# Kernel optimization log

Hardware: AMD Instinct MI355X
Metric: run time of the kernel (lower is better)

The kernel has to match this reference:

```python
import jax, jax.numpy as jnp
import numpy as np

N_Q = 16384; N_S = 16384; NN = 32; F_IN = 128; F_OUT = 256
K = 15; DIM = 3
RADIUS = 10.0
KP_EXTENT_CFG = 1.0      # config.NETWORK.KP_EXTENT (also scales learned offsets)
DENSITY = 5.0            # config.NETWORK.DENSITY_PARAMETER
EXTENT = KP_EXTENT_CFG * RADIUS / DENSITY   # 2.0
K_RADIUS = 1.5 * EXTENT
OFFSET_DIM = DIM * (K - 1)  # modulated=False, version=0 -> 42


def setup_inputs() -> dict:
    key = jax.random.key(0)
    ks = jax.random.split(key, 8)
    query_points = jax.random.uniform(ks[0], (N_Q, DIM), dtype=jnp.float32)
    support_points = jax.random.uniform(ks[1], (N_S, DIM), dtype=jnp.float32)
    neighbors = jax.random.randint(ks[2], (N_Q, NN), 0, N_S)
    features = jax.random.normal(ks[3], (N_S, F_IN), dtype=jnp.float32)
    # kernel points: fixed disposition inside ball of radius 1.5*extent, first point at center
    kp = jax.random.normal(ks[4], (K, DIM), dtype=jnp.float32)
    kp = kp / jnp.linalg.norm(kp, axis=1, keepdims=True) * (0.7 * K_RADIUS)
    K_points = kp.at[0].set(0.0)
    weight = jax.random.normal(ks[5], (K, F_IN, F_OUT), dtype=jnp.float32) / np.sqrt(F_IN)
    deformable_weight = jax.random.normal(ks[6], (K, F_IN, OFFSET_DIM), dtype=jnp.float32) / np.sqrt(F_IN)
    bias = jnp.zeros((OFFSET_DIM,), dtype=jnp.float32)
    return {"query_points": query_points, "support_points": support_points,
            "neighbors": neighbors, "features": features, "K_points": K_points,
            "weight": weight, "deformable_weight": deformable_weight, "bias": bias}


def _gather_neighb(query_points, support_points, neighbors, features):
    # pad with shadow point (far away) and zero feature row, as in KPConv_ops
    sp = jnp.concatenate([support_points, jnp.full((1, DIM), 1e6, support_points.dtype)], 0)
    ft = jnp.concatenate([features, jnp.zeros((1, features.shape[1]), features.dtype)], 0)
    rel = sp[neighbors] - query_points[:, None, :]   # [n, nn, 3]
    nfeat = ft[neighbors]                            # [n, nn, f]
    return rel, nfeat


def _linear_influence(sq_dist):
    # KP_INFLUENCE='linear': relu(1 - d/extent); CONVOLUTION_MODE='sum'
    return jnp.maximum(1.0 - jnp.sqrt(sq_dist) / EXTENT, 0.0)


def reference(query_points, support_points, neighbors, features, K_points,
              weight, deformable_weight, bias):
    rel, nfeat = _gather_neighb(query_points, support_points, neighbors, features)

    # --- rigid KPConv producing offsets (version=0) ---
    d0 = rel[:, :, None, :] - K_points[None, None, :, :]   # [n, nn, K, 3]
    sq0 = jnp.sum(d0 * d0, axis=-1)                        # [n, nn, K]
    w0 = _linear_influence(sq0)
    wf0 = jnp.einsum('enk,enf->ekf', w0, nfeat)            # [n, K, f]
    feat0 = jnp.einsum('ekf,kfo->eo', wf0, deformable_weight) + bias  # [n, 42]

    # not modulated: reshape to offsets, prepend zero offset for center kernel point
    offsets = feat0.reshape(-1, K - 1, DIM)
    offsets = jnp.concatenate([jnp.zeros_like(offsets[:, :1, :]), offsets], axis=1)
    offsets = offsets * KP_EXTENT_CFG                      # [n, K, 3]

    # --- deformable KPConv ---
    def_kp = K_points[None, :, :] + offsets                # [n, K, 3]
    d1 = rel[:, :, None, :] - def_kp[:, None, :, :]        # [n, nn, K, 3]
    sq1 = jnp.sum(d1 * d1, axis=-1)                        # [n, nn, K]
    w1 = _linear_influence(sq1)                            # out-of-range neighbors get 0 weight
    wf1 = jnp.einsum('enk,enf->ekf', w1, nfeat)            # [n, K, f]
    out = jnp.einsum('ekf,kfo->eo', wf1, weight)           # [n, f_out]
    return out
```

## Files before the change

kernel.cpp:

```cpp
#include <hip/hip_runtime.h>
#include <hip/hip_bf16.h>
#include <math.h>

typedef __attribute__((ext_vector_type(8))) short bf16x8;
typedef __attribute__((ext_vector_type(4))) float f32x4;

#define NQ 16384
#define NN 32
#define FI 128
#define FO 256
#define KPN 15
#define OD 42
#define INV_EXT 0.5f

#define KT2 64
#define WFA_STRIDE 2056

#define WS_DEFKP  0u
#define WS_FEATBF (3u * 1024u * 1024u)
#define WS_BSW    (7u * 1024u * 1024u)
#define WS_DWBH   (8u * 1024u * 1024u)
#define WS_DWBL   (WS_DWBH + 196608u)
#define WS_FEATPK (9u * 1024u * 1024u)

static __device__ __forceinline__ unsigned short f2bf(float x) {
    union { __hip_bfloat16 h; unsigned short u; } cv;
    cv.h = __float2bfloat16(x);
    return cv.u;
}
static __device__ __forceinline__ float bf2f(unsigned short h) {
    union { unsigned int u; float f; } cv;
    cv.u = ((unsigned int)h) << 16;
    return cv.f;
}

__global__ void prep_feat(const float* __restrict__ in,
                          unsigned short* __restrict__ fbf,
                          unsigned int* __restrict__ fpk) {
    const int i = (blockIdx.x * 256 + threadIdx.x) * 4;
    if (i >= NQ * FI) return;
    float4 a = *(const float4*)&in[i];
    unsigned short h0 = f2bf(a.x), h1 = f2bf(a.y), h2 = f2bf(a.z), h3 = f2bf(a.w);
    unsigned int* bp = (unsigned int*)&fbf[i];
    bp[0] = (unsigned int)h0 | ((unsigned int)h1 << 16);
    bp[1] = (unsigned int)h2 | ((unsigned int)h3 << 16);
    fpk[i + 0] = (unsigned int)h0 | ((unsigned int)f2bf(a.x - bf2f(h0)) << 16);
    fpk[i + 1] = (unsigned int)h1 | ((unsigned int)f2bf(a.y - bf2f(h1)) << 16);
    fpk[i + 2] = (unsigned int)h2 | ((unsigned int)f2bf(a.z - bf2f(h2)) << 16);
    fpk[i + 3] = (unsigned int)h3 | ((unsigned int)f2bf(a.w - bf2f(h3)) << 16);
}

__global__ void swz_B(const float* __restrict__ w, unsigned short* __restrict__ Bsw) {
    const int tid = blockIdx.x * 256 + threadIdx.x;
    const int lane = tid & 63;
    const int kt   = (tid >> 6) & 63;
    const int nt   = tid >> 12;
    const int n    = nt * 16 + (lane & 15);
    const int kbase = kt * 32 + (lane >> 4) * 8;
    unsigned int p[4];
    #pragma unroll
    for (int jj = 0; jj < 4; jj++) {
        unsigned int lo, hi;
        {
            const int kk = kbase + 2 * jj;
            const int f = kk >> 4, k = kk & 15;
            lo = (k < KPN) ? f2bf(w[(k * FI + f) * FO + n]) : 0u;
        }
        {
            const int kk = kbase + 2 * jj + 1;
            const int f = kk >> 4, k = kk & 15;
            hi = (k < KPN) ? f2bf(w[(k * FI + f) * FO + n]) : 0u;
        }
        p[jj] = lo | (hi << 16);
    }
    unsigned int* op = (unsigned int*)&Bsw[tid * 8];
    op[0] = p[0]; op[1] = p[1]; op[2] = p[2]; op[3] = p[3];
}

__global__ void build_dwB(const float* __restrict__ dw,
                          unsigned short* __restrict__ hi,
                          unsigned short* __restrict__ lo) {
    const int tid = blockIdx.x * 256 + threadIdx.x;
    if (tid >= 3 * 64 * 64) return;
    const int lane = tid & 63;
    const int kt   = (tid >> 6) & 63;
    const int nt   = tid >> 12;
    const int o    = nt * 16 + (lane & 15);
    const int kbase = kt * 32 + (lane >> 4) * 8;
    #pragma unroll
    for (int j = 0; j < 8; j++) {
        const int kf = kbase + j;
        const int f = kf >> 4, k = kf & 15;
        float v = (k < KPN && o < OD) ? dw[(k * FI + f) * OD + o] : 0.f;
        unsigned short h = f2bf(v);
        hi[tid * 8 + j] = h;
        lo[tid * 8 + j] = f2bf(v - bf2f(h));
    }
}

__global__ __launch_bounds__(512, 4)
void k1_offsets(const float* __restrict__ query, const float* __restrict__ support,
                const int* __restrict__ neighbors, const unsigned int* __restrict__ featpk,
                const float* __restrict__ kpoints,
                const unsigned short* __restrict__ dwB_hi,
                const unsigned short* __restrict__ dwB_lo,
                const float* __restrict__ bias, float* __restrict__ defkp)
{
    __shared__ unsigned short wfA_hi[8 * WFA_STRIDE];
    __shared__ unsigned short wfA_lo[8 * WFA_STRIDE];
    __shared__ float relx[256], rely[256], relz[256];
    __shared__ int   nbr_s[256];
    __shared__ float kp_s[48];
    __shared__ f32x4 cred[3 * 64];

    const int t = threadIdx.x;
    const int qbase = blockIdx.x * 8;
    if (t < 45) kp_s[t] = kpoints[t];
    if (t >= 45 && t < 48) kp_s[t] = 0.f;

    if (t < 256) {
        const int e = t >> 5, n = t & 31;
        const int q = qbase + e;
        const int idx = neighbors[q * NN + n];
        nbr_s[t] = idx;
        relx[t] = support[idx * 3 + 0] - query[q * 3 + 0];
        rely[t] = support[idx * 3 + 1] - query[q * 3 + 1];
        relz[t] = support[idx * 3 + 2] - query[q * 3 + 2];
    }
    __syncthreads();

    const int wave = t >> 6, lane = t & 63;
    const int quad = lane >> 4, low = lane & 15;

    {
        const int ee = wave;
        const int kb = (low < KPN) ? low * 3 : 0;
        const float kx = kp_s[kb + 0], ky = kp_s[kb + 1], kz = kp_s[kb + 2];
        union { unsigned short u[8]; bf16x8 v; } ah, al;
        int rows[8];
        #pragma unroll
        for (int j = 0; j < 8; j++) {
            const int ni = ee * 32 + quad * 8 + j;
            rows[j] = nbr_s[ni];
            const float dx = relx[ni] - kx;
            const float dy = rely[ni] - ky;
            const float dz = relz[ni] - kz;
            const float d = sqrtf(dx * dx + dy * dy + dz * dz);
            float w = 1.0f - d * INV_EXT;
            w = (low < KPN && w > 0.f) ? w : 0.f;
            const unsigned short h = f2bf(w);
            ah.u[j] = h;
            al.u[j] = f2bf(w - bf2f(h));
        }
        #pragma unroll
        for (int ft = 0; ft < 8; ft++) {
            union { unsigned int u[4]; bf16x8 v; } bh, bl;
            #pragma unroll
            for (int jj = 0; jj < 4; jj++) {
                const unsigned int d0 = featpk[rows[2 * jj] * FI + ft * 16 + low];
                const unsigned int d1 = featpk[rows[2 * jj + 1] * FI + ft * 16 + low];
                bh.u[jj] = __builtin_amdgcn_perm(d1, d0, 0x05040100u);
                bl.u[jj] = __builtin_amdgcn_perm(d1, d0, 0x07060302u);
            }
            f32x4 acc = {0.f, 0.f, 0.f, 0.f};
            acc = __builtin_amdgcn_mfma_f32_16x16x32_bf16(al.v, bh.v, acc, 0, 0, 0);
            acc = __builtin_amdgcn_mfma_f32_16x16x32_bf16(ah.v, bl.v, acc, 0, 0, 0);
            acc = __builtin_amdgcn_mfma_f32_16x16x32_bf16(ah.v, bh.v, acc, 0, 0, 0);
            const int kfb = (ft * 16 + low) * 16 + quad * 4;
            const unsigned short h0 = f2bf(acc[0]), h1 = f2bf(acc[1]);
            const unsigned short h2 = f2bf(acc[2]), h3 = f2bf(acc[3]);
            unsigned int* ph = (unsigned int*)&wfA_hi[ee * WFA_STRIDE + kfb];
            ph[0] = (unsigned int)h0 | ((unsigned int)h1 << 16);
            ph[1] = (unsigned int)h2 | ((unsigned int)h3 << 16);
            unsigned int* pl = (unsigned int*)&wfA_lo[ee * WFA_STRIDE + kfb];
            pl[0] = (unsigned int)f2bf(acc[0] - bf2f(h0)) |
                    ((unsigned int)f2bf(acc[1] - bf2f(h1)) << 16);
            pl[1] = (unsigned int)f2bf(acc[2] - bf2f(h2)) |
                    ((unsigned int)f2bf(acc[3] - bf2f(h3)) << 16);
        }
    }
    __syncthreads();

    f32x4 acc = {0.f, 0.f, 0.f, 0.f};
    const int nt = wave >> 1, half = wave & 1;
    if (wave < 6) {
        const bf16x8* Bh = (const bf16x8*)dwB_hi;
        const bf16x8* Bl = (const bf16x8*)dwB_lo;
        const int arow = (low & 7) * WFA_STRIDE;
        const int kt0 = half * 32;
        for (int kt = kt0; kt < kt0 + 32; kt++) {
            bf16x8 a_h = *(const bf16x8*)&wfA_hi[arow + kt * 32 + quad * 8];
            bf16x8 a_l = *(const bf16x8*)&wfA_lo[arow + kt * 32 + quad * 8];
            bf16x8 b_h = Bh[(nt * KT2 + kt) * 64 + lane];
            bf16x8 b_l = Bl[(nt * KT2 + kt) * 64 + lane];
            acc = __builtin_amdgcn_mfma_f32_16x16x32_bf16(a_l, b_h, acc, 0, 0, 0);
            acc = __builtin_amdgcn_mfma_f32_16x16x32_bf16(a_h, b_l, acc, 0, 0, 0);
            acc = __builtin_amdgcn_mfma_f32_16x16x32_bf16(a_h, b_h, acc, 0, 0, 0);
        }
        if (half == 1) cred[nt * 64 + lane] = acc;
    } else if (wave == 6 && lane < 24) {
        defkp[(qbase + lane / 3) * 45 + (lane % 3)] = kp_s[lane % 3];
    }
    __syncthreads();

    if (wave < 6 && half == 0) {
        f32x4 o2 = cred[nt * 64 + lane];
        acc[0] += o2[0]; acc[1] += o2[1]; acc[2] += o2[2]; acc[3] += o2[3];
        const int o = nt * 16 + low;
        if (quad < 2 && o < OD) {
            const float bo = bias[o] + kp_s[3 + o];
            #pragma unroll
            for (int r = 0; r < 4; r++) {
                const int ee = quad * 4 + r;
                defkp[(qbase + ee) * 45 + 3 + o] = bo + acc[r];
            }
        }
    }
}

__global__ __launch_bounds__(512, 4)
void k2_deform(const float* __restrict__ query, const float* __restrict__ support,
               const int* __restrict__ neighbors, const unsigned short* __restrict__ featbf,
               const unsigned short* __restrict__ Bsw, const float* __restrict__ defkp,
               float* __restrict__ out)
{
    __shared__ unsigned short wfA[16 * WFA_STRIDE];
    __shared__ float relx[512], rely[512], relz[512];
    __shared__ float dk_s[16 * 45];
    __shared__ int   nbr_s[512];

    const int t = threadIdx.x;
    const int qbase = blockIdx.x * 16;

    for (int i = t; i < 16 * 45; i += 512) dk_s[i] = defkp[qbase * 45 + i];

    const int e = t >> 5, n = t & 31;
    const int q = qbase + e;
    const int idx = neighbors[q * NN + n];
    nbr_s[t] = idx;
    relx[t] = support[idx * 3 + 0] - query[q * 3 + 0];
    rely[t] = support[idx * 3 + 1] - query[q * 3 + 1];
    relz[t] = support[idx * 3 + 2] - query[q * 3 + 2];
    __syncthreads();

    const int wave = t >> 6, lane = t & 63;
    const int quad = lane >> 4, low = lane & 15;

    {
        const int kb = (low < KPN) ? low * 3 : 0;
        for (int ei = 0; ei < 2; ei++) {
            const int ee = wave * 2 + ei;
            const float kx = dk_s[ee * 45 + kb + 0];
            const float ky = dk_s[ee * 45 + kb + 1];
            const float kz = dk_s[ee * 45 + kb + 2];
            union { unsigned short u[8]; bf16x8 v; } a;
            int rows[8];
            #pragma unroll
            for (int j = 0; j < 8; j++) {
                const int ni = ee * 32 + quad * 8 + j;
                rows[j] = nbr_s[ni];
                const float dx = relx[ni] - kx;
                const float dy = rely[ni] - ky;
                const float dz = relz[ni] - kz;
                const float d = sqrtf(dx * dx + dy * dy + dz * dz);
                float w = 1.0f - d * INV_EXT;
                w = (low < KPN && w > 0.f) ? w : 0.f;
                a.u[j] = f2bf(w);
            }
            #pragma unroll
            for (int ft = 0; ft < 8; ft++) {
                unsigned int p[4];
                #pragma unroll
                for (int j = 0; j < 4; j++) {
                    unsigned int lo2 = featbf[rows[2 * j] * FI + ft * 16 + low];
                    unsigned int hi2 = featbf[rows[2 * j + 1] * FI + ft * 16 + low];
                    p[j] = lo2 | (hi2 << 16);
                }
                bf16x8 b;
                {
                    union { unsigned int u[4]; bf16x8 v; } cv;
                    cv.u[0] = p[0]; cv.u[1] = p[1]; cv.u[2] = p[2]; cv.u[3] = p[3];
                    b = cv.v;
                }
                f32x4 acc = {0.f, 0.f, 0.f, 0.f};
                acc = __builtin_amdgcn_mfma_f32_16x16x32_bf16(a.v, b, acc, 0, 0, 0);
                const unsigned int w0 = (unsigned int)f2bf(acc[0]) | ((unsigned int)f2bf(acc[1]) << 16);
                const unsigned int w1 = (unsigned int)f2bf(acc[2]) | ((unsigned int)f2bf(acc[3]) << 16);
                unsigned short* wp = &wfA[ee * WFA_STRIDE + (ft * 16 + low) * 16 + quad * 4];
                ((unsigned int*)wp)[0] = w0;
                ((unsigned int*)wp)[1] = w1;
            }
        }
    }
    __syncthreads();

    {
        const int nt0 = wave * 2, nt1 = nt0 + 1;
        f32x4 acc0 = {0.f, 0.f, 0.f, 0.f}, acc1 = {0.f, 0.f, 0.f, 0.f};
        const bf16x8* Bp = (const bf16x8*)Bsw;
        bf16x8 a_c  = *(const bf16x8*)&wfA[low * WFA_STRIDE + quad * 8];
        bf16x8 b0_c = Bp[(nt0 * KT2) * 64 + lane];
        bf16x8 b1_c = Bp[(nt1 * KT2) * 64 + lane];
        for (int kt = 0; kt < KT2 - 1; kt++) {
            bf16x8 a_n  = *(const bf16x8*)&wfA[low * WFA_STRIDE + (kt + 1) * 32 + quad * 8];
            bf16x8 b0_n = Bp[(nt0 * KT2 + kt + 1) * 64 + lane];
            bf16x8 b1_n = Bp[(nt1 * KT2 + kt + 1) * 64 + lane];
            acc0 = __builtin_amdgcn_mfma_f32_16x16x32_bf16(a_c, b0_c, acc0, 0, 0, 0);
            acc1 = __builtin_amdgcn_mfma_f32_16x16x32_bf16(a_c, b1_c, acc1, 0, 0, 0);
            a_c = a_n; b0_c = b0_n; b1_c = b1_n;
        }
        acc0 = __builtin_amdgcn_mfma_f32_16x16x32_bf16(a_c, b0_c, acc0, 0, 0, 0);
        acc1 = __builtin_amdgcn_mfma_f32_16x16x32_bf16(a_c, b1_c, acc1, 0, 0, 0);
        #pragma unroll
        for (int r = 0; r < 4; r++) {
            const int ee = quad * 4 + r;
            out[(qbase + ee) * FO + nt0 * 16 + low] = acc0[r];
            out[(qbase + ee) * FO + nt1 * 16 + low] = acc1[r];
        }
    }
}

extern "C" void kernel_launch(void* const* d_in, const int* in_sizes, int n_in,
                              void* d_out, int out_size, void* d_ws, size_t ws_size,
                              hipStream_t stream) {
    const float* query     = (const float*)d_in[0];
    const float* support   = (const float*)d_in[1];
    const int*   neighbors = (const int*)  d_in[2];
    const float* features  = (const float*)d_in[3];
    const float* kpoints   = (const float*)d_in[4];
    const float* weight    = (const float*)d_in[5];
    const float* dweight   = (const float*)d_in[6];
    const float* bias      = (const float*)d_in[7];
    float*       out       = (float*)d_out;

    char* ws = (char*)d_ws;
    float*          defkp  = (float*)(ws + WS_DEFKP);
    unsigned short* featbf = (unsigned short*)(ws + WS_FEATBF);
    unsigned short* Bsw    = (unsigned short*)(ws + WS_BSW);
    unsigned short* dwBh   = (unsigned short*)(ws + WS_DWBH);
    unsigned short* dwBl   = (unsigned short*)(ws + WS_DWBL);
    unsigned int*   featpk = (unsigned int*)(ws + WS_FEATPK);

    prep_feat<<<(NQ * FI / 4 + 255) / 256, 256, 0, stream>>>(features, featbf, featpk);
    build_dwB<<<48, 256, 0, stream>>>(dweight, dwBh, dwBl);
    swz_B<<<256, 256, 0, stream>>>(weight, Bsw);

    k1_offsets<<<NQ / 8, 512, 0, stream>>>(query, support, neighbors, featpk,
                                           kpoints, dwBh, dwBl, bias, defkp);
    k2_deform<<<NQ / 16, 512, 0, stream>>>(query, support, neighbors, featbf,
                                           Bsw, defkp, out);
}
```

Measured before the change: 194.6 us.

## Fuse offset and deformable KPConv kernels, cache gathered features in registers

Merges the three preprocessing kernels into one launch and fuses the offset-producing KPConv with the deformable KPConv in a single kernel. Deformed kernel points stay in shared memory, and the gathered bf16 feature fragments stay in registers so the second stage does not gather them again. This removes the defkp round trip through global memory, the separate bf16 feature copy, and two launches. In exchange the fused kernel holds 32 extra registers per thread, which may hurt occupancy. The final GEMM now runs on 8 queries per block (half the MFMA rows wasted) instead of 16, which halves reuse of the B weights per block.

```diff
diff --git a/kernel.cpp b/kernel.cpp
--- a/kernel.cpp
+++ b/kernel.cpp
@@ -16,12 +16,10 @@
 #define KT2 64
 #define WFA_STRIDE 2056
 
-#define WS_DEFKP  0u
-#define WS_FEATBF (3u * 1024u * 1024u)
-#define WS_BSW    (7u * 1024u * 1024u)
-#define WS_DWBH   (8u * 1024u * 1024u)
+#define WS_FEATPK 0u
+#define WS_BSW    (8u * 1024u * 1024u)
+#define WS_DWBH   (9u * 1024u * 1024u)
 #define WS_DWBL   (WS_DWBH + 196608u)
-#define WS_FEATPK (9u * 1024u * 1024u)
 
 static __device__ __forceinline__ unsigned short f2bf(float x) {
     union { __hip_bfloat16 h; unsigned short u; } cv;
@@ -34,77 +32,72 @@
     return cv.f;
 }
 
-__global__ void prep_feat(const float* __restrict__ in,
-                          unsigned short* __restrict__ fbf,
-                          unsigned int* __restrict__ fpk) {
-    const int i = (blockIdx.x * 256 + threadIdx.x) * 4;
-    if (i >= NQ * FI) return;
-    float4 a = *(const float4*)&in[i];
-    unsigned short h0 = f2bf(a.x), h1 = f2bf(a.y), h2 = f2bf(a.z), h3 = f2bf(a.w);
-    unsigned int* bp = (unsigned int*)&fbf[i];
-    bp[0] = (unsigned int)h0 | ((unsigned int)h1 << 16);
-    bp[1] = (unsigned int)h2 | ((unsigned int)h3 << 16);
-    fpk[i + 0] = (unsigned int)h0 | ((unsigned int)f2bf(a.x - bf2f(h0)) << 16);
-    fpk[i + 1] = (unsigned int)h1 | ((unsigned int)f2bf(a.y - bf2f(h1)) << 16);
-    fpk[i + 2] = (unsigned int)h2 | ((unsigned int)f2bf(a.z - bf2f(h2)) << 16);
-    fpk[i + 3] = (unsigned int)h3 | ((unsigned int)f2bf(a.w - bf2f(h3)) << 16);
-}
-
-__global__ void swz_B(const float* __restrict__ w, unsigned short* __restrict__ Bsw) {
-    const int tid = blockIdx.x * 256 + threadIdx.x;
-    const int lane = tid & 63;
-    const int kt   = (tid >> 6) & 63;
-    const int nt   = tid >> 12;
-    const int n    = nt * 16 + (lane & 15);
-    const int kbase = kt * 32 + (lane >> 4) * 8;
-    unsigned int p[4];
-    #pragma unroll
-    for (int jj = 0; jj < 4; jj++) {
-        unsigned int lo, hi;
-        {
-            const int kk = kbase + 2 * jj;
-            const int f = kk >> 4, k = kk & 15;
-            lo = (k < KPN) ? f2bf(w[(k * FI + f) * FO + n]) : 0u;
-        }
-        {
-            const int kk = kbase + 2 * jj + 1;
-            const int f = kk >> 4, k = kk & 15;
-            hi = (k < KPN) ? f2bf(w[(k * FI + f) * FO + n]) : 0u;
-        }
-        p[jj] = lo | (hi << 16);
-    }
-    unsigned int* op = (unsigned int*)&Bsw[tid * 8];
-    op[0] = p[0]; op[1] = p[1]; op[2] = p[2]; op[3] = p[3];
-}
-
-__global__ void build_dwB(const float* __restrict__ dw,
-                          unsigned short* __restrict__ hi,
-                          unsigned short* __restrict__ lo) {
-    const int tid = blockIdx.x * 256 + threadIdx.x;
-    if (tid >= 3 * 64 * 64) return;
-    const int lane = tid & 63;
-    const int kt   = (tid >> 6) & 63;
-    const int nt   = tid >> 12;
-    const int o    = nt * 16 + (lane & 15);
-    const int kbase = kt * 32 + (lane >> 4) * 8;
-    #pragma unroll
-    for (int j = 0; j < 8; j++) {
-        const int kf = kbase + j;
-        const int f = kf >> 4, k = kf & 15;
-        float v = (k < KPN && o < OD) ? dw[(k * FI + f) * OD + o] : 0.f;
-        unsigned short h = f2bf(v);
-        hi[tid * 8 + j] = h;
-        lo[tid * 8 + j] = f2bf(v - bf2f(h));
+__global__ void pre_all(const float* __restrict__ feat, unsigned int* __restrict__ fpk,
+                        const float* __restrict__ w, unsigned short* __restrict__ Bsw,
+                        const float* __restrict__ dw,
+                        unsigned short* __restrict__ dhi, unsigned short* __restrict__ dlo)
+{
+    const int b = blockIdx.x, t = threadIdx.x;
+    if (b < 2048) {
+        const int i = (b * 256 + t) * 4;
+        float4 a = *(const float4*)&feat[i];
+        unsigned short h0 = f2bf(a.x), h1 = f2bf(a.y), h2 = f2bf(a.z), h3 = f2bf(a.w);
+        fpk[i + 0] = (unsigned int)h0 | ((unsigned int)f2bf(a.x - bf2f(h0)) << 16);
+        fpk[i + 1] = (unsigned int)h1 | ((unsigned int)f2bf(a.y - bf2f(h1)) << 16);
+        fpk[i + 2] = (unsigned int)h2 | ((unsigned int)f2bf(a.z - bf2f(h2)) << 16);
+        fpk[i + 3] = (unsigned int)h3 | ((unsigned int)f2bf(a.w - bf2f(h3)) << 16);
+    } else if (b < 2048 + 256) {
+        const int tid = (b - 2048) * 256 + t;
+        const int lane = tid & 63;
+        const int kt   = (tid >> 6) & 63;
+        const int nt   = tid >> 12;
+        const int n    = nt * 16 + (lane & 15);
+        const int kbase = kt * 32 + (lane >> 4) * 8;
+        unsigned int p[4];
+        #pragma unroll
+        for (int jj = 0; jj < 4; jj++) {
+            unsigned int lo, hi;
+            {
+                const int kk = kbase + 2 * jj;
+                const int f = kk >> 4, k = kk & 15;
+                lo = (k < KPN) ? f2bf(w[(k * FI + f) * FO + n]) : 0u;
+            }
+            {
+                const int kk = kbase + 2 * jj + 1;
+                const int f = kk >> 4, k = kk & 15;
+                hi = (k < KPN) ? f2bf(w[(k * FI + f) * FO + n]) : 0u;
+            }
+            p[jj] = lo | (hi << 16);
+        }
+        unsigned int* op = (unsigned int*)&Bsw[tid * 8];
+        op[0] = p[0]; op[1] = p[1]; op[2] = p[2]; op[3] = p[3];
+    } else {
+        const int tid = (b - 2304) * 256 + t;
+        const int lane = tid & 63;
+        const int kt   = (tid >> 6) & 63;
+        const int nt   = tid >> 12;
+        const int o    = nt * 16 + (lane & 15);
+        const int kbase = kt * 32 + (lane >> 4) * 8;
+        #pragma unroll
+        for (int j = 0; j < 8; j++) {
+            const int kf = kbase + j;
+            const int f = kf >> 4, k = kf & 15;
+            float v = (k < KPN && o < OD) ? dw[(k * FI + f) * OD + o] : 0.f;
+            unsigned short h = f2bf(v);
+            dhi[tid * 8 + j] = h;
+            dlo[tid * 8 + j] = f2bf(v - bf2f(h));
+        }
     }
 }
 
 __global__ __launch_bounds__(512, 4)
-void k1_offsets(const float* __restrict__ query, const float* __restrict__ support,
-                const int* __restrict__ neighbors, const unsigned int* __restrict__ featpk,
-                const float* __restrict__ kpoints,
-                const unsigned short* __restrict__ dwB_hi,
-                const unsigned short* __restrict__ dwB_lo,
-                const float* __restrict__ bias, float* __restrict__ defkp)
+void k_fused(const float* __restrict__ query, const float* __restrict__ support,
+             const int* __restrict__ neighbors, const unsigned int* __restrict__ featpk,
+             const float* __restrict__ kpoints,
+             const unsigned short* __restrict__ dwB_hi,
+             const unsigned short* __restrict__ dwB_lo,
+             const unsigned short* __restrict__ Bsw,
+             const float* __restrict__ bias, float* __restrict__ out)
 {
     __shared__ unsigned short wfA_hi[8 * WFA_STRIDE];
     __shared__ unsigned short wfA_lo[8 * WFA_STRIDE];
@@ -112,6 +105,7 @@
     __shared__ int   nbr_s[256];
     __shared__ float kp_s[48];
     __shared__ f32x4 cred[3 * 64];
+    __shared__ float dk_s[8 * 45];
 
     const int t = threadIdx.x;
     const int qbase = blockIdx.x * 8;
@@ -131,10 +125,12 @@
 
     const int wave = t >> 6, lane = t & 63;
     const int quad = lane >> 4, low = lane & 15;
+    const int kb = (low < KPN) ? low * 3 : 0;
+
+    unsigned int bhc[8][4];
 
     {
         const int ee = wave;
-        const int kb = (low < KPN) ? low * 3 : 0;
         const float kx = kp_s[kb + 0], ky = kp_s[kb + 1], kz = kp_s[kb + 2];
         union { unsigned short u[8]; bf16x8 v; } ah, al;
         int rows[8];
@@ -161,6 +157,7 @@
                 const unsigned int d1 = featpk[rows[2 * jj + 1] * FI + ft * 16 + low];
                 bh.u[jj] = __builtin_amdgcn_perm(d1, d0, 0x05040100u);
                 bl.u[jj] = __builtin_amdgcn_perm(d1, d0, 0x07060302u);
+                bhc[ft][jj] = bh.u[jj];
             }
             f32x4 acc = {0.f, 0.f, 0.f, 0.f};
             acc = __builtin_amdgcn_mfma_f32_16x16x32_bf16(al.v, bh.v, acc, 0, 0, 0);
@@ -181,141 +178,95 @@
     }
     __syncthreads();
 
-    f32x4 acc = {0.f, 0.f, 0.f, 0.f};
-    const int nt = wave >> 1, half = wave & 1;
-    if (wave < 6) {
-        const bf16x8* Bh = (const bf16x8*)dwB_hi;
-        const bf16x8* Bl = (const bf16x8*)dwB_lo;
+    {
+        f32x4 acc = {0.f, 0.f, 0.f, 0.f};
+        const int nt = wave >> 1, half = wave & 1;
+        if (wave < 6) {
+            const bf16x8* Bh = (const bf16x8*)dwB_hi;
+            const bf16x8* Bl = (const bf16x8*)dwB_lo;
+            const int arow = (low & 7) * WFA_STRIDE;
+            const int kt0 = half * 32;
+            for (int kt = kt0; kt < kt0 + 32; kt++) {
+                bf16x8 a_h = *(const bf16x8*)&wfA_hi[arow + kt * 32 + quad * 8];
+                bf16x8 a_l = *(const bf16x8*)&wfA_lo[arow + kt * 32 + quad * 8];
+                bf16x8 b_h = Bh[(nt * KT2 + kt) * 64 + lane];
+                bf16x8 b_l = Bl[(nt * KT2 + kt) * 64 + lane];
+                acc = __builtin_amdgcn_mfma_f32_16x16x32_bf16(a_l, b_h, acc, 0, 0, 0);
+                acc = __builtin_amdgcn_mfma_f32_16x16x32_bf16(a_h, b_l, acc, 0, 0, 0);
+                acc = __builtin_amdgcn_mfma_f32_16x16x32_bf16(a_h, b_h, acc, 0, 0, 0);
+            }
+            if (half == 1) cred[nt * 64 + lane] = acc;
+        } else if (wave == 6 && lane < 24) {
+            dk_s[(lane / 3) * 45 + (lane % 3)] = kp_s[lane % 3];
+        }
+        __syncthreads();
+        if (wave < 6 && half == 0) {
+            f32x4 o2 = cred[nt * 64 + lane];
+            acc[0] += o2[0]; acc[1] += o2[1]; acc[2] += o2[2]; acc[3] += o2[3];
+            const int o = nt * 16 + low;
+            if (quad < 2 && o < OD) {
+                const float bo = bias[o] + kp_s[3 + o];
+                #pragma unroll
+                for (int r = 0; r < 4; r++) {
+                    const int ee = quad * 4 + r;
+                    dk_s[ee * 45 + 3 + o] = bo + acc[r];
+                }
+            }
+        }
+    }
+    __syncthreads();
+
+    {
+        const int ee = wave;
+        const float kx = dk_s[ee * 45 + kb + 0];
+        const float ky = dk_s[ee * 45 + kb + 1];
+        const float kz = dk_s[ee * 45 + kb + 2];
+        union { unsigned short u[8]; bf16x8 v; } a1;
+        #pragma unroll
+        for (int j = 0; j < 8; j++) {
+            const int ni = ee * 32 + quad * 8 + j;
+            const float dx = relx[ni] - kx;
+            const float dy = rely[ni] - ky;
+            const float dz = relz[ni] - kz;
+            const float d = sqrtf(dx * dx + dy * dy + dz * dz);
+            float w = 1.0f - d * INV_EXT;
+            w = (low < KPN && w > 0.f) ? w : 0.f;
+            a1.u[j] = f2bf(w);
+        }
+        #pragma unroll
+        for (int ft = 0; ft < 8; ft++) {
+            union { unsigned int u[4]; bf16x8 v; } b;
+            b.u[0] = bhc[ft][0]; b.u[1] = bhc[ft][1];
+            b.u[2] = bhc[ft][2]; b.u[3] = bhc[ft][3];
+            f32x4 acc = {0.f, 0.f, 0.f, 0.f};
+            acc = __builtin_amdgcn_mfma_f32_16x16x32_bf16(a1.v, b.v, acc, 0, 0, 0);
+            const int kfb = (ft * 16 + low) * 16 + quad * 4;
+            unsigned int* wp = (unsigned int*)&wfA_hi[ee * WFA_STRIDE + kfb];
+            wp[0] = (unsigned int)f2bf(acc[0]) | ((unsigned int)f2bf(acc[1]) << 16);
+            wp[1] = (unsigned int)f2bf(acc[2]) | ((unsigned int)f2bf(acc[3]) << 16);
+        }
+    }
+    __syncthreads();
+
+    {
+        const int nt0 = wave * 2, nt1 = nt0 + 1;
+        f32x4 acc0 = {0.f, 0.f, 0.f, 0.f}, acc1 = {0.f, 0.f, 0.f, 0.f};
+        const bf16x8* Bp = (const bf16x8*)Bsw;
         const int arow = (low & 7) * WFA_STRIDE;
-        const int kt0 = half * 32;
-        for (int kt = kt0; kt < kt0 + 32; kt++) {
-            bf16x8 a_h = *(const bf16x8*)&wfA_hi[arow + kt * 32 + quad * 8];
-            bf16x8 a_l = *(const bf16x8*)&wfA_lo[arow + kt * 32 + quad * 8];
-            bf16x8 b_h = Bh[(nt * KT2 + kt) * 64 + lane];
-            bf16x8 b_l = Bl[(nt * KT2 + kt) * 64 + lane];
-            acc = __builtin_amdgcn_mfma_f32_16x16x32_bf16(a_l, b_h, acc, 0, 0, 0);
-            acc = __builtin_amdgcn_mfma_f32_16x16x32_bf16(a_h, b_l, acc, 0, 0, 0);
-            acc = __builtin_amdgcn_mfma_f32_16x16x32_bf16(a_h, b_h, acc, 0, 0, 0);
-        }
-        if (half == 1) cred[nt * 64 + lane] = acc;
-    } else if (wave == 6 && lane < 24) {
-        defkp[(qbase + lane / 3) * 45 + (lane % 3)] = kp_s[lane % 3];
-    }
-    __syncthreads();
-
-    if (wave < 6 && half == 0) {
-        f32x4 o2 = cred[nt * 64 + lane];
-        acc[0] += o2[0]; acc[1] += o2[1]; acc[2] += o2[2]; acc[3] += o2[3];
-        const int o = nt * 16 + low;
-        if (quad < 2 && o < OD) {
-            const float bo = bias[o] + kp_s[3 + o];
+        for (int kt = 0; kt < KT2; kt++) {
+            bf16x8 a  = *(const bf16x8*)&wfA_hi[arow + kt * 32 + quad * 8];
+            bf16x8 b0 = Bp[(nt0 * KT2 + kt) * 64 + lane];
+            bf16x8 b1 = Bp[(nt1 * KT2 + kt) * 64 + lane];
+            acc0 = __builtin_amdgcn_mfma_f32_16x16x32_bf16(a, b0, acc0, 0, 0, 0);
+            acc1 = __builtin_amdgcn_mfma_f32_16x16x32_bf16(a, b1, acc1, 0, 0, 0);
+        }
+        if (quad < 2) {
             #pragma unroll
             for (int r = 0; r < 4; r++) {
                 const int ee = quad * 4 + r;
-                defkp[(qbase + ee) * 45 + 3 + o] = bo + acc[r];
-            }
-        }
-    }
-}
-
-__global__ __launch_bounds__(512, 4)
-void k2_deform(const float* __restrict__ query, const float* __restrict__ support,
-               const int* __restrict__ neighbors, const unsigned short* __restrict__ featbf,
-               const unsigned short* __restrict__ Bsw, const float* __restrict__ defkp,
-               float* __restrict__ out)
-{
-    __shared__ unsigned short wfA[16 * WFA_STRIDE];
-    __shared__ float relx[512], rely[512], relz[512];
-    __shared__ float dk_s[16 * 45];
-    __shared__ int   nbr_s[512];
-
-    const int t = threadIdx.x;
-    const int qbase = blockIdx.x * 16;
-
-    for (int i = t; i < 16 * 45; i += 512) dk_s[i] = defkp[qbase * 45 + i];
-
-    const int e = t >> 5, n = t & 31;
-    const int q = qbase + e;
-    const int idx = neighbors[q * NN + n];
-    nbr_s[t] = idx;
-    relx[t] = support[idx * 3 + 0] - query[q * 3 + 0];
-    rely[t] = support[idx * 3 + 1] - query[q * 3 + 1];
-    relz[t] = support[idx * 3 + 2] - query[q * 3 + 2];
-    __syncthreads();
-
-    const int wave = t >> 6, lane = t & 63;
-    const int quad = lane >> 4, low = lane & 15;
-
-    {
-        const int kb = (low < KPN) ? low * 3 : 0;
-        for (int ei = 0; ei < 2; ei++) {
-            const int ee = wave * 2 + ei;
-            const float kx = dk_s[ee * 45 + kb + 0];
-            const float ky = dk_s[ee * 45 + kb + 1];
-            const float kz = dk_s[ee * 45 + kb + 2];
-            union { unsigned short u[8]; bf16x8 v; } a;
-            int rows[8];
-            #pragma unroll
-            for (int j = 0; j < 8; j++) {
-                const int ni = ee * 32 + quad * 8 + j;
-                rows[j] = nbr_s[ni];
-                const float dx = relx[ni] - kx;
-                const float dy = rely[ni] - ky;
-                const float dz = relz[ni] - kz;
-                const float d = sqrtf(dx * dx + dy * dy + dz * dz);
-                float w = 1.0f - d * INV_EXT;
-                w = (low < KPN && w > 0.f) ? w : 0.f;
-                a.u[j] = f2bf(w);
-            }
-            #pragma unroll
-            for (int ft = 0; ft < 8; ft++) {
-                unsigned int p[4];
-                #pragma unroll
-                for (int j = 0; j < 4; j++) {
-                    unsigned int lo2 = featbf[rows[2 * j] * FI + ft * 16 + low];
-                    unsigned int hi2 = featbf[rows[2 * j + 1] * FI + ft * 16 + low];
-                    p[j] = lo2 | (hi2 << 16);
-                }
-                bf16x8 b;
-                {
-                    union { unsigned int u[4]; bf16x8 v; } cv;
-                    cv.u[0] = p[0]; cv.u[1] = p[1]; cv.u[2] = p[2]; cv.u[3] = p[3];
-                    b = cv.v;
-                }
-                f32x4 acc = {0.f, 0.f, 0.f, 0.f};
-                acc = __builtin_amdgcn_mfma_f32_16x16x32_bf16(a.v, b, acc, 0, 0, 0);
-                const unsigned int w0 = (unsigned int)f2bf(acc[0]) | ((unsigned int)f2bf(acc[1]) << 16);
-                const unsigned int w1 = (unsigned int)f2bf(acc[2]) | ((unsigned int)f2bf(acc[3]) << 16);
-                unsigned short* wp = &wfA[ee * WFA_STRIDE + (ft * 16 + low) * 16 + quad * 4];
-                ((unsigned int*)wp)[0] = w0;
-                ((unsigned int*)wp)[1] = w1;
-            }
-        }
-    }
-    __syncthreads();
-
-    {
-        const int nt0 = wave * 2, nt1 = nt0 + 1;
-        f32x4 acc0 = {0.f, 0.f, 0.f, 0.f}, acc1 = {0.f, 0.f, 0.f, 0.f};
-        const bf16x8* Bp = (const bf16x8*)Bsw;
-        bf16x8 a_c  = *(const bf16x8*)&wfA[low * WFA_STRIDE + quad * 8];
-        bf16x8 b0_c = Bp[(nt0 * KT2) * 64 + lane];
-        bf16x8 b1_c = Bp[(nt1 * KT2) * 64 + lane];
-        for (int kt = 0; kt < KT2 - 1; kt++) {
-            bf16x8 a_n  = *(const bf16x8*)&wfA[low * WFA_STRIDE + (kt + 1) * 32 + quad * 8];
-            bf16x8 b0_n = Bp[(nt0 * KT2 + kt + 1) * 64 + lane];
-            bf16x8 b1_n = Bp[(nt1 * KT2 + kt + 1) * 64 + lane];
-            acc0 = __builtin_amdgcn_mfma_f32_16x16x32_bf16(a_c, b0_c, acc0, 0, 0, 0);
-            acc1 = __builtin_amdgcn_mfma_f32_16x16x32_bf16(a_c, b1_c, acc1, 0, 0, 0);
-            a_c = a_n; b0_c = b0_n; b1_c = b1_n;
-        }
-        acc0 = __builtin_amdgcn_mfma_f32_16x16x32_bf16(a_c, b0_c, acc0, 0, 0, 0);
-        acc1 = __builtin_amdgcn_mfma_f32_16x16x32_bf16(a_c, b1_c, acc1, 0, 0, 0);
-        #pragma unroll
-        for (int r = 0; r < 4; r++) {
-            const int ee = quad * 4 + r;
-            out[(qbase + ee) * FO + nt0 * 16 + low] = acc0[r];
-            out[(qbase + ee) * FO + nt1 * 16 + low] = acc1[r];
+                out[(qbase + ee) * FO + nt0 * 16 + low] = acc0[r];
+                out[(qbase + ee) * FO + nt1 * 16 + low] = acc1[r];
+            }
         }
     }
 }
@@ -334,19 +285,13 @@
     float*       out       = (float*)d_out;
 
     char* ws = (char*)d_ws;
-    float*          defkp  = (float*)(ws + WS_DEFKP);
-    unsigned short* featbf = (unsigned short*)(ws + WS_FEATBF);
+    unsigned int*   featpk = (unsigned int*)(ws + WS_FEATPK);
     unsigned short* Bsw    = (unsigned short*)(ws + WS_BSW);
     unsigned short* dwBh   = (unsigned short*)(ws + WS_DWBH);
     unsigned short* dwBl   = (unsigned short*)(ws + WS_DWBL);
-    unsigned int*   featpk = (unsigned int*)(ws + WS_FEATPK);
-
-    prep_feat<<<(NQ * FI / 4 + 255) / 256, 256, 0, stream>>>(features, featbf, featpk);
-    build_dwB<<<48, 256, 0, stream>>>(dweight, dwBh, dwBl);
-    swz_B<<<256, 256, 0, stream>>>(weight, Bsw);
-
-    k1_offsets<<<NQ / 8, 512, 0, stream>>>(query, support, neighbors, featpk,
-                                           kpoints, dwBh, dwBl, bias, defkp);
-    k2_deform<<<NQ / 16, 512, 0, stream>>>(query, support, neighbors, featbf,
-                                           Bsw, defkp, out);
-}
+
+    pre_all<<<2352, 256, 0, stream>>>(features, featpk, weight, Bsw,
+                                      dweight, dwBh, dwBl);
+    k_fused<<<NQ / 8, 512, 0, stream>>>(query, support, neighbors, featpk,
+                                        kpoints, dwBh, dwBl, Bsw, bias, out);
+}
```

After: 212.3 us. 9.1% more time.

## Merge prep kernels, drop bf16 feature copy, and XOR-swizzle LDS tiles

Applied to the files above, without the earlier changes.

The three preprocessing kernels become one launch, and the separate bf16 feature buffer is removed, so k2 now gathers from the packed hi/lo array and extracts the hi half with a byte-permute. The padded LDS stride of 2056 is replaced by an unpadded 2048 stride with an XOR swizzle of 32-element blocks by row, meant to avoid bank conflicts on both the stores and the MFMA A-operand loads. This saves a kernel launch and one write of the feature array, but k2's gathers now read 4-byte words where they read 2-byte ones, doubling that gather traffic.

```diff
diff --git a/kernel.cpp b/kernel.cpp
--- a/kernel.cpp
+++ b/kernel.cpp
@@ -14,14 +14,15 @@
 #define INV_EXT 0.5f
 
 #define KT2 64
-#define WFA_STRIDE 2056
-
-#define WS_DEFKP  0u
-#define WS_FEATBF (3u * 1024u * 1024u)
-#define WS_BSW    (7u * 1024u * 1024u)
-#define WS_DWBH   (8u * 1024u * 1024u)
+#define WST 2048
+
+#define SWZ(row, blk) (((blk) ^ ((row) & 7)) << 5)
+
+#define WS_FEATPK 0u
+#define WS_BSW    (8u * 1024u * 1024u)
+#define WS_DWBH   (9u * 1024u * 1024u)
 #define WS_DWBL   (WS_DWBH + 196608u)
-#define WS_FEATPK (9u * 1024u * 1024u)
+#define WS_DEFKP  (10u * 1024u * 1024u)
 
 static __device__ __forceinline__ unsigned short f2bf(float x) {
     union { __hip_bfloat16 h; unsigned short u; } cv;
@@ -34,67 +35,61 @@
     return cv.f;
 }
 
-__global__ void prep_feat(const float* __restrict__ in,
-                          unsigned short* __restrict__ fbf,
-                          unsigned int* __restrict__ fpk) {
-    const int i = (blockIdx.x * 256 + threadIdx.x) * 4;
-    if (i >= NQ * FI) return;
-    float4 a = *(const float4*)&in[i];
-    unsigned short h0 = f2bf(a.x), h1 = f2bf(a.y), h2 = f2bf(a.z), h3 = f2bf(a.w);
-    unsigned int* bp = (unsigned int*)&fbf[i];
-    bp[0] = (unsigned int)h0 | ((unsigned int)h1 << 16);
-    bp[1] = (unsigned int)h2 | ((unsigned int)h3 << 16);
-    fpk[i + 0] = (unsigned int)h0 | ((unsigned int)f2bf(a.x - bf2f(h0)) << 16);
-    fpk[i + 1] = (unsigned int)h1 | ((unsigned int)f2bf(a.y - bf2f(h1)) << 16);
-    fpk[i + 2] = (unsigned int)h2 | ((unsigned int)f2bf(a.z - bf2f(h2)) << 16);
-    fpk[i + 3] = (unsigned int)h3 | ((unsigned int)f2bf(a.w - bf2f(h3)) << 16);
-}
-
-__global__ void swz_B(const float* __restrict__ w, unsigned short* __restrict__ Bsw) {
-    const int tid = blockIdx.x * 256 + threadIdx.x;
-    const int lane = tid & 63;
-    const int kt   = (tid >> 6) & 63;
-    const int nt   = tid >> 12;
-    const int n    = nt * 16 + (lane & 15);
-    const int kbase = kt * 32 + (lane >> 4) * 8;
-    unsigned int p[4];
-    #pragma unroll
-    for (int jj = 0; jj < 4; jj++) {
-        unsigned int lo, hi;
-        {
-            const int kk = kbase + 2 * jj;
-            const int f = kk >> 4, k = kk & 15;
-            lo = (k < KPN) ? f2bf(w[(k * FI + f) * FO + n]) : 0u;
-        }
-        {
-            const int kk = kbase + 2 * jj + 1;
-            const int f = kk >> 4, k = kk & 15;
-            hi = (k < KPN) ? f2bf(w[(k * FI + f) * FO + n]) : 0u;
-        }
-        p[jj] = lo | (hi << 16);
-    }
-    unsigned int* op = (unsigned int*)&Bsw[tid * 8];
-    op[0] = p[0]; op[1] = p[1]; op[2] = p[2]; op[3] = p[3];
-}
-
-__global__ void build_dwB(const float* __restrict__ dw,
-                          unsigned short* __restrict__ hi,
-                          unsigned short* __restrict__ lo) {
-    const int tid = blockIdx.x * 256 + threadIdx.x;
-    if (tid >= 3 * 64 * 64) return;
-    const int lane = tid & 63;
-    const int kt   = (tid >> 6) & 63;
-    const int nt   = tid >> 12;
-    const int o    = nt * 16 + (lane & 15);
-    const int kbase = kt * 32 + (lane >> 4) * 8;
-    #pragma unroll
-    for (int j = 0; j < 8; j++) {
-        const int kf = kbase + j;
-        const int f = kf >> 4, k = kf & 15;
-        float v = (k < KPN && o < OD) ? dw[(k * FI + f) * OD + o] : 0.f;
-        unsigned short h = f2bf(v);
-        hi[tid * 8 + j] = h;
-        lo[tid * 8 + j] = f2bf(v - bf2f(h));
+__global__ void pre_all(const float* __restrict__ feat, unsigned int* __restrict__ fpk,
+                        const float* __restrict__ w, unsigned short* __restrict__ Bsw,
+                        const float* __restrict__ dw,
+                        unsigned short* __restrict__ dhi, unsigned short* __restrict__ dlo)
+{
+    const int b = blockIdx.x, t = threadIdx.x;
+    if (b < 2048) {
+        const int i = (b * 256 + t) * 4;
+        float4 a = *(const float4*)&feat[i];
+        unsigned short h0 = f2bf(a.x), h1 = f2bf(a.y), h2 = f2bf(a.z), h3 = f2bf(a.w);
+        fpk[i + 0] = (unsigned int)h0 | ((unsigned int)f2bf(a.x - bf2f(h0)) << 16);
+        fpk[i + 1] = (unsigned int)h1 | ((unsigned int)f2bf(a.y - bf2f(h1)) << 16);
+        fpk[i + 2] = (unsigned int)h2 | ((unsigned int)f2bf(a.z - bf2f(h2)) << 16);
+        fpk[i + 3] = (unsigned int)h3 | ((unsigned int)f2bf(a.w - bf2f(h3)) << 16);
+    } else if (b < 2048 + 256) {
+        const int tid = (b - 2048) * 256 + t;
+        const int lane = tid & 63;
+        const int kt   = (tid >> 6) & 63;
+        const int nt   = tid >> 12;
+        const int n    = nt * 16 + (lane & 15);
+        const int kbase = kt * 32 + (lane >> 4) * 8;
+        unsigned int p[4];
+        #pragma unroll
+        for (int jj = 0; jj < 4; jj++) {
+            unsigned int lo, hi;
+            {
+                const int kk = kbase + 2 * jj;
+                const int f = kk >> 4, k = kk & 15;
+                lo = (k < KPN) ? f2bf(w[(k * FI + f) * FO + n]) : 0u;
+            }
+            {
+                const int kk = kbase + 2 * jj + 1;
+                const int f = kk >> 4, k = kk & 15;
+                hi = (k < KPN) ? f2bf(w[(k * FI + f) * FO + n]) : 0u;
+            }
+            p[jj] = lo | (hi << 16);
+        }
+        unsigned int* op = (unsigned int*)&Bsw[tid * 8];
+        op[0] = p[0]; op[1] = p[1]; op[2] = p[2]; op[3] = p[3];
+    } else {
+        const int tid = (b - 2304) * 256 + t;
+        const int lane = tid & 63;
+        const int kt   = (tid >> 6) & 63;
+        const int nt   = tid >> 12;
+        const int o    = nt * 16 + (lane & 15);
+        const int kbase = kt * 32 + (lane >> 4) * 8;
+        #pragma unroll
+        for (int j = 0; j < 8; j++) {
+            const int kf = kbase + j;
+            const int f = kf >> 4, k = kf & 15;
+            float v = (k < KPN && o < OD) ? dw[(k * FI + f) * OD + o] : 0.f;
+            unsigned short h = f2bf(v);
+            dhi[tid * 8 + j] = h;
+            dlo[tid * 8 + j] = f2bf(v - bf2f(h));
+        }
     }
 }
 
@@ -106,8 +101,8 @@
                 const unsigned short* __restrict__ dwB_lo,
                 const float* __restrict__ bias, float* __restrict__ defkp)
 {
-    __shared__ unsigned short wfA_hi[8 * WFA_STRIDE];
-    __shared__ unsigned short wfA_lo[8 * WFA_STRIDE];
+    __shared__ unsigned short wfA_hi[8 * WST];
+    __shared__ unsigned short wfA_lo[8 * WST];
     __shared__ float relx[256], rely[256], relz[256];
     __shared__ int   nbr_s[256];
     __shared__ float kp_s[48];
@@ -166,13 +161,14 @@
             acc = __builtin_amdgcn_mfma_f32_16x16x32_bf16(al.v, bh.v, acc, 0, 0, 0);
             acc = __builtin_amdgcn_mfma_f32_16x16x32_bf16(ah.v, bl.v, acc, 0, 0, 0);
             acc = __builtin_amdgcn_mfma_f32_16x16x32_bf16(ah.v, bh.v, acc, 0, 0, 0);
-            const int kfb = (ft * 16 + low) * 16 + quad * 4;
+            const int col  = ft * 16 + low;
+            const int base = ee * WST + SWZ(ee, col >> 1) + ((col & 1) << 4) + quad * 4;
             const unsigned short h0 = f2bf(acc[0]), h1 = f2bf(acc[1]);
             const unsigned short h2 = f2bf(acc[2]), h3 = f2bf(acc[3]);
-            unsigned int* ph = (unsigned int*)&wfA_hi[ee * WFA_STRIDE + kfb];
+            unsigned int* ph = (unsigned int*)&wfA_hi[base];
             ph[0] = (unsigned int)h0 | ((unsigned int)h1 << 16);
             ph[1] = (unsigned int)h2 | ((unsigned int)h3 << 16);
-            unsigned int* pl = (unsigned int*)&wfA_lo[ee * WFA_STRIDE + kfb];
+            unsigned int* pl = (unsigned int*)&wfA_lo[base];
             pl[0] = (unsigned int)f2bf(acc[0] - bf2f(h0)) |
                     ((unsigned int)f2bf(acc[1] - bf2f(h1)) << 16);
             pl[1] = (unsigned int)f2bf(acc[2] - bf2f(h2)) |
@@ -186,11 +182,13 @@
     if (wave < 6) {
         const bf16x8* Bh = (const bf16x8*)dwB_hi;
         const bf16x8* Bl = (const bf16x8*)dwB_lo;
-        const int arow = (low & 7) * WFA_STRIDE;
+        const int rl = low & 7;
+        const int arow = rl * WST;
         const int kt0 = half * 32;
         for (int kt = kt0; kt < kt0 + 32; kt++) {
-            bf16x8 a_h = *(const bf16x8*)&wfA_hi[arow + kt * 32 + quad * 8];
-            bf16x8 a_l = *(const bf16x8*)&wfA_lo[arow + kt * 32 + quad * 8];
+            const int ao = arow + SWZ(rl, kt) + quad * 8;
+            bf16x8 a_h = *(const bf16x8*)&wfA_hi[ao];
+            bf16x8 a_l = *(const bf16x8*)&wfA_lo[ao];
             bf16x8 b_h = Bh[(nt * KT2 + kt) * 64 + lane];
             bf16x8 b_l = Bl[(nt * KT2 + kt) * 64 + lane];
             acc = __builtin_amdgcn_mfma_f32_16x16x32_bf16(a_l, b_h, acc, 0, 0, 0);
@@ -220,11 +218,11 @@
 
 __global__ __launch_bounds__(512, 4)
 void k2_deform(const float* __restrict__ query, const float* __restrict__ support,
-               const int* __restrict__ neighbors, const unsigned short* __restrict__ featbf,
+               const int* __restrict__ neighbors, const unsigned int* __restrict__ featpk,
                const unsigned short* __restrict__ Bsw, const float* __restrict__ defkp,
                float* __restrict__ out)
 {
-    __shared__ unsigned short wfA[16 * WFA_STRIDE];
+    __shared__ unsigned short wfA[16 * WST];
     __shared__ float relx[512], rely[512], relz[512];
     __shared__ float dk_s[16 * 45];
     __shared__ int   nbr_s[512];
@@ -269,26 +267,20 @@
             }
             #pragma unroll
             for (int ft = 0; ft < 8; ft++) {
-                unsigned int p[4];
+                union { unsigned int u[4]; bf16x8 v; } b;
                 #pragma unroll
-                for (int j = 0; j < 4; j++) {
-                    unsigned int lo2 = featbf[rows[2 * j] * FI + ft * 16 + low];
-                    unsigned int hi2 = featbf[rows[2 * j + 1] * FI + ft * 16 + low];
-                    p[j] = lo2 | (hi2 << 16);
-                }
-                bf16x8 b;
-                {
-                    union { unsigned int u[4]; bf16x8 v; } cv;
-                    cv.u[0] = p[0]; cv.u[1] = p[1]; cv.u[2] = p[2]; cv.u[3] = p[3];
-                    b = cv.v;
+                for (int jj = 0; jj < 4; jj++) {
+                    const unsigned int d0 = featpk[rows[2 * jj] * FI + ft * 16 + low];
+                    const unsigned int d1 = featpk[rows[2 * jj + 1] * FI + ft * 16 + low];
+                    b.u[jj] = __builtin_amdgcn_perm(d1, d0, 0x05040100u);
                 }
                 f32x4 acc = {0.f, 0.f, 0.f, 0.f};
-                acc = __builtin_amdgcn_mfma_f32_16x16x32_bf16(a.v, b, acc, 0, 0, 0);
-                const unsigned int w0 = (unsigned int)f2bf(acc[0]) | ((unsigned int)f2bf(acc[1]) << 16);
-                const unsigned int w1 = (unsigned int)f2bf(acc[2]) | ((unsigned int)f2bf(acc[3]) << 16);
-                unsigned short* wp = &wfA[ee * WFA_STRIDE + (ft * 16 + low) * 16 + quad * 4];
-                ((unsigned int*)wp)[0] = w0;
-                ((unsigned int*)wp)[1] = w1;
+                acc = __builtin_amdgcn_mfma_f32_16x16x32_bf16(a.v, b.v, acc, 0, 0, 0);
+                const int col  = ft * 16 + low;
+                const int base = ee * WST + SWZ(ee, col >> 1) + ((col & 1) << 4) + quad * 4;
+                unsigned int* wp = (unsigned int*)&wfA[base];
+                wp[0] = (unsigned int)f2bf(acc[0]) | ((unsigned int)f2bf(acc[1]) << 16);
+                wp[1] = (unsigned int)f2bf(acc[2]) | ((unsigned int)f2bf(acc[3]) << 16);
             }
         }
     }
@@ -298,11 +290,12 @@
         const int nt0 = wave * 2, nt1 = nt0 + 1;
         f32x4 acc0 = {0.f, 0.f, 0.f, 0.f}, acc1 = {0.f, 0.f, 0.f, 0.f};
         const bf16x8* Bp = (const bf16x8*)Bsw;
-        bf16x8 a_c  = *(const bf16x8*)&wfA[low * WFA_STRIDE + quad * 8];
+        const int arow = low * WST;
+        bf16x8 a_c  = *(const bf16x8*)&wfA[arow + SWZ(low, 0) + quad * 8];
         bf16x8 b0_c = Bp[(nt0 * KT2) * 64 + lane];
         bf16x8 b1_c = Bp[(nt1 * KT2) * 64 + lane];
         for (int kt = 0; kt < KT2 - 1; kt++) {
-            bf16x8 a_n  = *(const bf16x8*)&wfA[low * WFA_STRIDE + (kt + 1) * 32 + quad * 8];
+            bf16x8 a_n  = *(const bf16x8*)&wfA[arow + SWZ(low, kt + 1) + quad * 8];
             bf16x8 b0_n = Bp[(nt0 * KT2 + kt + 1) * 64 + lane];
             bf16x8 b1_n = Bp[(nt1 * KT2 + kt + 1) * 64 + lane];
             acc0 = __builtin_amdgcn_mfma_f32_16x16x32_bf16(a_c, b0_c, acc0, 0, 0, 0);
@@ -334,19 +327,16 @@
     float*       out       = (float*)d_out;
 
     char* ws = (char*)d_ws;
-    float*          defkp  = (float*)(ws + WS_DEFKP);
-    unsigned short* featbf = (unsigned short*)(ws + WS_FEATBF);
+    unsigned int*   featpk = (unsigned int*)(ws + WS_FEATPK);
     unsigned short* Bsw    = (unsigned short*)(ws + WS_BSW);
     unsigned short* dwBh   = (unsigned short*)(ws + WS_DWBH);
     unsigned short* dwBl   = (unsigned short*)(ws + WS_DWBL);
-    unsigned int*   featpk = (unsigned int*)(ws + WS_FEATPK);
-
-    prep_feat<<<(NQ * FI / 4 + 255) / 256, 256, 0, stream>>>(features, featbf, featpk);
-    build_dwB<<<48, 256, 0, stream>>>(dweight, dwBh, dwBl);
-    swz_B<<<256, 256, 0, stream>>>(weight, Bsw);
-
+    float*          defkp  = (float*)(ws + WS_DEFKP);
+
+    pre_all<<<2352, 256, 0, stream>>>(features, featpk, weight, Bsw,
+                                      dweight, dwBh, dwBl);
     k1_offsets<<<NQ / 8, 512, 0, stream>>>(query, support, neighbors, featpk,
                                            kpoints, dwBh, dwBl, bias, defkp);
-    k2_deform<<<NQ / 16, 512, 0, stream>>>(query, support, neighbors, featbf,
+    k2_deform<<<NQ / 16, 512, 0, stream>>>(query, support, neighbors, featpk,
                                            Bsw, defkp, out);
 }
```

Measured after the change: 197.2 us. Within noise of the previous version (+1.3%).
